# Optimization experiments

Measured on AMD Instinct MI355X. Metric: run time of the kernel, lower is better.

## Reference

```python
import jax, jax.numpy as jnp
import numpy as np
from jax import lax

B, T, I = 8192, 784, 1
H, C = 30, 10


def setup_inputs() -> dict:
    key = jax.random.key(0)
    ks = jax.random.split(key, 6)
    inputs = jax.random.normal(ks[0], (B, T, I), dtype=jnp.float32)
    # RNN cell params (expRNN-style modReLU cell): input kernel (no bias),
    # recurrent kernel (no bias), modReLU bias.
    W_ih = jax.random.normal(ks[1], (H, I), dtype=jnp.float32) / np.sqrt(I)
    W_hh = jax.random.normal(ks[2], (H, H), dtype=jnp.float32) / np.sqrt(H)
    b_mod = jax.random.normal(ks[3], (H,), dtype=jnp.float32) * 0.01
    # Final classifier Linear(hidden_size, num_classes)
    W_lin = jax.random.normal(ks[4], (C, H), dtype=jnp.float32) / np.sqrt(H)
    b_lin = jax.random.normal(ks[5], (C,), dtype=jnp.float32) * 0.01
    return {"inputs": inputs, "W_ih": W_ih, "W_hh": W_hh, "b_mod": b_mod,
            "W_lin": W_lin, "b_lin": b_lin}


def _modrelu(z, b):
    # modReLU: sign(z) * relu(|z| + b)
    return jnp.sign(z) * jax.nn.relu(jnp.abs(z) + b)


def reference(inputs, W_ih, W_hh, b_mod, W_lin, b_lin):
    # inputs: [B, T, 1]; recurrence over T with hidden state [B, H]
    xs = jnp.swapaxes(inputs, 0, 1)  # [T, B, I]

    def step(h, x_t):
        z = x_t @ W_ih.T + h @ W_hh.T  # [B, H]
        h_new = _modrelu(z, b_mod)
        return h_new, None

    h0 = jnp.zeros((inputs.shape[0], W_hh.shape[0]), dtype=inputs.dtype)
    h_final, _ = lax.scan(step, h0, xs)
    return h_final @ W_lin.T + b_lin  # [B, C] logits
```

## Files before the change

### kernel.cpp

```cpp
#include <hip/hip_runtime.h>


#define T_STEPS 784
#define NBATCH  8192
#define NH      30
#define NC      10
#define BPW     16
#define XPAD    788

typedef short bf16x8 __attribute__((ext_vector_type(8)));
typedef float f32x4  __attribute__((ext_vector_type(4)));
typedef unsigned int u32x4 __attribute__((ext_vector_type(4)));

#define MFMA(acc, a, b) \
    acc = __builtin_amdgcn_mfma_f32_16x16x32_bf16(a, b, acc, 0, 0, 0)

__device__ __forceinline__ float truncbf(float x) {
    return __int_as_float(__float_as_int(x) & 0xFFFF0000);
}
__device__ __forceinline__ unsigned pk2(float lo, float hi) {
    return __builtin_amdgcn_perm(__float_as_uint(hi), __float_as_uint(lo),
                                 0x07060302u);
}
__device__ __forceinline__ bf16x8 pk8(float a0, float a1, float a2, float a3,
                                      float a4, float a5, float a6, float a7) {
    u32x4 u = { pk2(a0, a1), pk2(a2, a3), pk2(a4, a5), pk2(a6, a7) };
    return __builtin_bit_cast(bf16x8, u);
}
__device__ __forceinline__ float modrelu(float z, float b) {
    return copysignf(fmaxf(fabsf(z) + b, 0.0f), z);
}

__global__ __launch_bounds__(64, 1)
void rnn_modrelu_mfma2(const float* __restrict__ inp,
                       const float* __restrict__ W_ih,
                       const float* __restrict__ W_hh,
                       const float* __restrict__ b_mod,
                       const float* __restrict__ W_lin,
                       const float* __restrict__ b_lin,
                       float* __restrict__ out)
{
    __shared__ __align__(16) float xl[BPW * XPAD];
    __shared__ float hf[BPW * 32];

    const int l   = threadIdx.x;
    const int blk = blockIdx.x;
    const int m   = l & 15;
    const int q   = l >> 4;

    {
        const float4* src = (const float4*)(inp + (size_t)blk * (BPW * T_STEPS));
        #pragma unroll
        for (int k = 0; k < 49; ++k) {
            int v = l + 64 * k;
            if (v < (BPW * T_STEPS) / 4) {
                int b   = v / 196;
                int rem = v - b * 196;
                *(float4*)(xl + b * XPAD + 4 * rem) = src[v];
            }
        }
    }

    bf16x8 afr[2][3];
    #pragma unroll
    for (int g = 0; g < 2; ++g) {
        const int row = 8 * (m >> 2) + (m & 3) + 4 * g;
        float wv[8], r1v[8], r2v[8];
        #pragma unroll
        for (int j = 0; j < 8; ++j) {
            const int col = q * 8 + j;
            float v = (row < NH && col < NH) ? W_hh[row * NH + col] : 0.0f;
            wv[j]  = v;
            r1v[j] = v - truncbf(v);
            r2v[j] = r1v[j] - truncbf(r1v[j]);
        }
        afr[g][0] = pk8(wv[0],  wv[1],  wv[2],  wv[3],  wv[4],  wv[5],  wv[6],  wv[7]);
        afr[g][1] = pk8(r1v[0], r1v[1], r1v[2], r1v[3], r1v[4], r1v[5], r1v[6], r1v[7]);
        afr[g][2] = pk8(r2v[0], r2v[1], r2v[2], r2v[3], r2v[4], r2v[5], r2v[6], r2v[7]);
    }

    float bm[8], wih[8];
    #pragma unroll
    for (int i = 0; i < 8; ++i) {
        const int row = 8 * q + i;
        bm[i]  = (row < NH) ? b_mod[row] : 0.0f;
        wih[i] = (row < NH) ? W_ih[row]  : 0.0f;
    }

    __syncthreads();

    const float* xb = xl + m * XPAD;
    float xcur = xb[0];
    float xnx  = (T_STEPS > 1) ? xb[1] : xb[0];

    bf16x8 bf1 = {0,0,0,0,0,0,0,0};
    bf16x8 bf2 = {0,0,0,0,0,0,0,0};
    bf16x8 bf3 = {0,0,0,0,0,0,0,0};
    float hv[8];
    #pragma unroll
    for (int i = 0; i < 8; ++i) hv[i] = 0.0f;

    #pragma unroll 1
    for (int t = 0; t < T_STEPS; ++t) {
        int tf = t + 2; if (tf >= T_STEPS) tf = T_STEPS - 1;
        const float xf = xb[tf];

        f32x4 c0, c1;
        #pragma unroll
        for (int i = 0; i < 4; ++i) {
            c0[i] = wih[i]     * xcur;
            c1[i] = wih[4 + i] * xcur;
        }

        MFMA(c0, afr[0][0], bf1);  MFMA(c1, afr[1][0], bf1);
        MFMA(c0, afr[0][1], bf1);  MFMA(c1, afr[1][1], bf1);
        MFMA(c0, afr[0][2], bf1);  MFMA(c1, afr[1][2], bf1);
        MFMA(c0, afr[0][0], bf2);  MFMA(c1, afr[1][0], bf2);
        MFMA(c0, afr[0][1], bf2);  MFMA(c1, afr[1][1], bf2);
        MFMA(c0, afr[0][0], bf3);  MFMA(c1, afr[1][0], bf3);

        #pragma unroll
        for (int i = 0; i < 4; ++i) {
            hv[i]     = modrelu(c0[i], bm[i]);
            hv[4 + i] = modrelu(c1[i], bm[4 + i]);
        }

        float r1[8], r2[8];
        #pragma unroll
        for (int j = 0; j < 8; ++j) {
            r1[j] = hv[j] - truncbf(hv[j]);
            r2[j] = r1[j] - truncbf(r1[j]);
        }
        bf1 = pk8(hv[0], hv[1], hv[2], hv[3], hv[4], hv[5], hv[6], hv[7]);
        bf2 = pk8(r1[0], r1[1], r1[2], r1[3], r1[4], r1[5], r1[6], r1[7]);
        bf3 = pk8(r2[0], r2[1], r2[2], r2[3], r2[4], r2[5], r2[6], r2[7]);

        xcur = xnx;
        xnx  = xf;
    }

    #pragma unroll
    for (int i = 0; i < 8; ++i) {
        const int row = 8 * q + i;
        if (row < NH) hf[m * 32 + row] = hv[i];
    }
    __syncthreads();

    #pragma unroll
    for (int it = 0; it < 3; ++it) {
        const int k = l + 64 * it;
        if (k < BPW * NC) {
            const int b = k / NC;
            const int c = k % NC;
            float acc = b_lin[c];
            #pragma unroll
            for (int i = 0; i < NH; ++i) {
                acc = fmaf(W_lin[c * NH + i], hf[b * 32 + i], acc);
            }
            out[((size_t)blk * BPW + b) * NC + c] = acc;
        }
    }
}

extern "C" void kernel_launch(void* const* d_in, const int* in_sizes, int n_in,
                              void* d_out, int out_size, void* d_ws, size_t ws_size,
                              hipStream_t stream) {
    const float* inp   = (const float*)d_in[0];
    const float* W_ih  = (const float*)d_in[1];
    const float* W_hh  = (const float*)d_in[2];
    const float* b_mod = (const float*)d_in[3];
    const float* W_lin = (const float*)d_in[4];
    const float* b_lin = (const float*)d_in[5];
    float* out = (float*)d_out;

    dim3 grid(NBATCH / BPW);
    dim3 block(64);
    rnn_modrelu_mfma2<<<grid, block, 0, stream>>>(inp, W_ih, W_hh, b_mod,
                                                  W_lin, b_lin, out);
}
```

Measured before the change: 305.0 us.

## Split hidden rows across two waves with LDS exchange of hidden state

```diff
diff --git a/kernel.cpp b/kernel.cpp
--- a/kernel.cpp
+++ b/kernel.cpp
@@ -11,48 +11,52 @@
 typedef short bf16x8 __attribute__((ext_vector_type(8)));
 typedef float f32x4  __attribute__((ext_vector_type(4)));
 typedef unsigned int u32x4 __attribute__((ext_vector_type(4)));
+typedef unsigned int u32x2 __attribute__((ext_vector_type(2)));
 
 #define MFMA(acc, a, b) \
     acc = __builtin_amdgcn_mfma_f32_16x16x32_bf16(a, b, acc, 0, 0, 0)
 
-__device__ __forceinline__ float truncbf(float x) {
+static __device__ __forceinline__ float truncbf(float x) {
     return __int_as_float(__float_as_int(x) & 0xFFFF0000);
 }
-__device__ __forceinline__ unsigned pk2(float lo, float hi) {
+static __device__ __forceinline__ unsigned pk2(float lo, float hi) {
     return __builtin_amdgcn_perm(__float_as_uint(hi), __float_as_uint(lo),
                                  0x07060302u);
 }
-__device__ __forceinline__ bf16x8 pk8(float a0, float a1, float a2, float a3,
-                                      float a4, float a5, float a6, float a7) {
-    u32x4 u = { pk2(a0, a1), pk2(a2, a3), pk2(a4, a5), pk2(a6, a7) };
+static __device__ __forceinline__ bf16x8 pk8(const float* v) {
+    u32x4 u = { pk2(v[0], v[1]), pk2(v[2], v[3]),
+                pk2(v[4], v[5]), pk2(v[6], v[7]) };
     return __builtin_bit_cast(bf16x8, u);
 }
-__device__ __forceinline__ float modrelu(float z, float b) {
+static __device__ __forceinline__ float modrelu(float z, float b) {
     return copysignf(fmaxf(fabsf(z) + b, 0.0f), z);
 }
 
-__global__ __launch_bounds__(64, 1)
-void rnn_modrelu_mfma2(const float* __restrict__ inp,
-                       const float* __restrict__ W_ih,
-                       const float* __restrict__ W_hh,
-                       const float* __restrict__ b_mod,
-                       const float* __restrict__ W_lin,
-                       const float* __restrict__ b_lin,
-                       float* __restrict__ out)
+__global__ __launch_bounds__(128, 1)
+void rnn_rowsplit(const float* __restrict__ inp,
+                  const float* __restrict__ W_ih,
+                  const float* __restrict__ W_hh,
+                  const float* __restrict__ b_mod,
+                  const float* __restrict__ W_lin,
+                  const float* __restrict__ b_lin,
+                  float* __restrict__ out)
 {
     __shared__ __align__(16) float xl[BPW * XPAD];
-    __shared__ float hf[BPW * 32];
+    __shared__ __align__(16) unsigned ex[2][3][4][16][4];
+    __shared__ __align__(16) float hf[BPW * 36];
 
-    const int l   = threadIdx.x;
-    const int blk = blockIdx.x;
+    const int tid = threadIdx.x;
+    const int g   = tid >> 6;
+    const int l   = tid & 63;
     const int m   = l & 15;
     const int q   = l >> 4;
+    const int blk = blockIdx.x;
 
     {
         const float4* src = (const float4*)(inp + (size_t)blk * (BPW * T_STEPS));
         #pragma unroll
-        for (int k = 0; k < 49; ++k) {
-            int v = l + 64 * k;
+        for (int k = 0; k < 25; ++k) {
+            int v = tid + 128 * k;
             if (v < (BPW * T_STEPS) / 4) {
                 int b   = v / 196;
                 int rem = v - b * 196;
@@ -61,9 +65,8 @@
         }
     }
 
-    bf16x8 afr[2][3];
-    #pragma unroll
-    for (int g = 0; g < 2; ++g) {
+    bf16x8 a1, a2, a3;
+    {
         const int row = 8 * (m >> 2) + (m & 3) + 4 * g;
         float wv[8], r1v[8], r2v[8];
         #pragma unroll
@@ -74,15 +77,13 @@
             r1v[j] = v - truncbf(v);
             r2v[j] = r1v[j] - truncbf(r1v[j]);
         }
-        afr[g][0] = pk8(wv[0],  wv[1],  wv[2],  wv[3],  wv[4],  wv[5],  wv[6],  wv[7]);
-        afr[g][1] = pk8(r1v[0], r1v[1], r1v[2], r1v[3], r1v[4], r1v[5], r1v[6], r1v[7]);
-        afr[g][2] = pk8(r2v[0], r2v[1], r2v[2], r2v[3], r2v[4], r2v[5], r2v[6], r2v[7]);
+        a1 = pk8(wv); a2 = pk8(r1v); a3 = pk8(r2v);
     }
 
-    float bm[8], wih[8];
+    float bm[4], wih[4];
     #pragma unroll
-    for (int i = 0; i < 8; ++i) {
-        const int row = 8 * q + i;
+    for (int i = 0; i < 4; ++i) {
+        const int row = 8 * q + 4 * g + i;
         bm[i]  = (row < NH) ? b_mod[row] : 0.0f;
         wih[i] = (row < NH) ? W_ih[row]  : 0.0f;
     }
@@ -91,71 +92,69 @@
 
     const float* xb = xl + m * XPAD;
     float xcur = xb[0];
-    float xnx  = (T_STEPS > 1) ? xb[1] : xb[0];
+    float xnx  = xb[1];
 
-    bf16x8 bf1 = {0,0,0,0,0,0,0,0};
-    bf16x8 bf2 = {0,0,0,0,0,0,0,0};
-    bf16x8 bf3 = {0,0,0,0,0,0,0,0};
-    float hv[8];
-    #pragma unroll
-    for (int i = 0; i < 8; ++i) hv[i] = 0.0f;
+    bf16x8 bf1 = {}, bf2 = {}, bf3 = {};
+    float hv[4] = {0.0f, 0.0f, 0.0f, 0.0f};
 
-    #pragma unroll 1
+    unsigned* const wr0 = &ex[0][0][q][m][2 * g];
+    unsigned* const wr1 = &ex[1][0][q][m][2 * g];
+    const unsigned* const rd0 = &ex[0][0][q][m][0];
+    const unsigned* const rd1 = &ex[1][0][q][m][0];
+
+    #pragma unroll 2
     for (int t = 0; t < T_STEPS; ++t) {
         int tf = t + 2; if (tf >= T_STEPS) tf = T_STEPS - 1;
         const float xf = xb[tf];
 
-        f32x4 c0, c1;
+        f32x4 ca, cb;
+        #pragma unroll
+        for (int i = 0; i < 4; ++i) ca[i] = wih[i] * xcur;
+        cb = (f32x4){0.0f, 0.0f, 0.0f, 0.0f};
+
+        MFMA(ca, a1, bf1);   MFMA(cb, a2, bf1);
+        MFMA(ca, a3, bf1);   MFMA(cb, a1, bf2);
+        MFMA(ca, a2, bf2);   MFMA(cb, a1, bf3);
+
+        #pragma unroll
+        for (int i = 0; i < 4; ++i) hv[i] = modrelu(ca[i] + cb[i], bm[i]);
+
+        float r1[4], r2[4];
         #pragma unroll
         for (int i = 0; i < 4; ++i) {
-            c0[i] = wih[i]     * xcur;
-            c1[i] = wih[4 + i] * xcur;
+            r1[i] = hv[i] - truncbf(hv[i]);
+            r2[i] = r1[i] - truncbf(r1[i]);
         }
 
-        MFMA(c0, afr[0][0], bf1);  MFMA(c1, afr[1][0], bf1);
-        MFMA(c0, afr[0][1], bf1);  MFMA(c1, afr[1][1], bf1);
-        MFMA(c0, afr[0][2], bf1);  MFMA(c1, afr[1][2], bf1);
-        MFMA(c0, afr[0][0], bf2);  MFMA(c1, afr[1][0], bf2);
-        MFMA(c0, afr[0][1], bf2);  MFMA(c1, afr[1][1], bf2);
-        MFMA(c0, afr[0][0], bf3);  MFMA(c1, afr[1][0], bf3);
+        unsigned* w = (t & 1) ? wr1 : wr0;
+        *(u32x2*)(w +   0) = (u32x2){ pk2(hv[0], hv[1]), pk2(hv[2], hv[3]) };
+        *(u32x2*)(w + 256) = (u32x2){ pk2(r1[0], r1[1]), pk2(r1[2], r1[3]) };
+        *(u32x2*)(w + 512) = (u32x2){ pk2(r2[0], r2[1]), pk2(r2[2], r2[3]) };
 
-        #pragma unroll
-        for (int i = 0; i < 4; ++i) {
-            hv[i]     = modrelu(c0[i], bm[i]);
-            hv[4 + i] = modrelu(c1[i], bm[4 + i]);
-        }
+        __syncthreads();
 
-        float r1[8], r2[8];
-        #pragma unroll
-        for (int j = 0; j < 8; ++j) {
-            r1[j] = hv[j] - truncbf(hv[j]);
-            r2[j] = r1[j] - truncbf(r1[j]);
-        }
-        bf1 = pk8(hv[0], hv[1], hv[2], hv[3], hv[4], hv[5], hv[6], hv[7]);
-        bf2 = pk8(r1[0], r1[1], r1[2], r1[3], r1[4], r1[5], r1[6], r1[7]);
-        bf3 = pk8(r2[0], r2[1], r2[2], r2[3], r2[4], r2[5], r2[6], r2[7]);
+        const unsigned* r = (t & 1) ? rd1 : rd0;
+        bf1 = __builtin_bit_cast(bf16x8, *(const u32x4*)(r + 0));
+        bf2 = __builtin_bit_cast(bf16x8, *(const u32x4*)(r + 256));
+        bf3 = __builtin_bit_cast(bf16x8, *(const u32x4*)(r + 512));
 
-        xcur = xnx;
-        xnx  = xf;
+        xcur = xnx; xnx = xf;
     }
 
-    #pragma unroll
-    for (int i = 0; i < 8; ++i) {
-        const int row = 8 * q + i;
-        if (row < NH) hf[m * 32 + row] = hv[i];
-    }
+    *(float4*)(hf + m * 36 + 8 * q + 4 * g) =
+        make_float4(hv[0], hv[1], hv[2], hv[3]);
     __syncthreads();
 
     #pragma unroll
-    for (int it = 0; it < 3; ++it) {
-        const int k = l + 64 * it;
+    for (int it = 0; it < 2; ++it) {
+        const int k = tid + 128 * it;
         if (k < BPW * NC) {
             const int b = k / NC;
             const int c = k % NC;
             float acc = b_lin[c];
             #pragma unroll
             for (int i = 0; i < NH; ++i) {
-                acc = fmaf(W_lin[c * NH + i], hf[b * 32 + i], acc);
+                acc = fmaf(W_lin[c * NH + i], hf[b * 36 + i], acc);
             }
             out[((size_t)blk * BPW + b) * NC + c] = acc;
         }
@@ -174,7 +173,7 @@
     float* out = (float*)d_out;
 
     dim3 grid(NBATCH / BPW);
-    dim3 block(64);
-    rnn_modrelu_mfma2<<<grid, block, 0, stream>>>(inp, W_ih, W_hh, b_mod,
-                                                  W_lin, b_lin, out);
+    dim3 block(128);
+    rnn_rowsplit<<<grid, block, 0, stream>>>(inp, W_ih, W_hh, b_mod,
+                                             W_lin, b_lin, out);
 }
```

New measurement: 266.3 us. 12.7% less time.

## Interleave two batch streams per wave and split MFMA accumulator chains

Applied to the files above, without the earlier changes.

```diff
diff --git a/kernel.cpp b/kernel.cpp
--- a/kernel.cpp
+++ b/kernel.cpp
@@ -5,7 +5,8 @@
 #define NBATCH  8192
 #define NH      30
 #define NC      10
-#define BPW     16
+#define NS      2
+#define BPW     32
 #define XPAD    788
 
 typedef short bf16x8 __attribute__((ext_vector_type(8)));
@@ -15,33 +16,33 @@
 #define MFMA(acc, a, b) \
     acc = __builtin_amdgcn_mfma_f32_16x16x32_bf16(a, b, acc, 0, 0, 0)
 
-__device__ __forceinline__ float truncbf(float x) {
+static __device__ __forceinline__ float truncbf(float x) {
     return __int_as_float(__float_as_int(x) & 0xFFFF0000);
 }
-__device__ __forceinline__ unsigned pk2(float lo, float hi) {
+static __device__ __forceinline__ unsigned pk2(float lo, float hi) {
     return __builtin_amdgcn_perm(__float_as_uint(hi), __float_as_uint(lo),
                                  0x07060302u);
 }
-__device__ __forceinline__ bf16x8 pk8(float a0, float a1, float a2, float a3,
-                                      float a4, float a5, float a6, float a7) {
-    u32x4 u = { pk2(a0, a1), pk2(a2, a3), pk2(a4, a5), pk2(a6, a7) };
+static __device__ __forceinline__ bf16x8 pk8(const float* v) {
+    u32x4 u = { pk2(v[0], v[1]), pk2(v[2], v[3]),
+                pk2(v[4], v[5]), pk2(v[6], v[7]) };
     return __builtin_bit_cast(bf16x8, u);
 }
-__device__ __forceinline__ float modrelu(float z, float b) {
+static __device__ __forceinline__ float modrelu(float z, float b) {
     return copysignf(fmaxf(fabsf(z) + b, 0.0f), z);
 }
 
 __global__ __launch_bounds__(64, 1)
-void rnn_modrelu_mfma2(const float* __restrict__ inp,
-                       const float* __restrict__ W_ih,
-                       const float* __restrict__ W_hh,
-                       const float* __restrict__ b_mod,
-                       const float* __restrict__ W_lin,
-                       const float* __restrict__ b_lin,
-                       float* __restrict__ out)
+void rnn_2stream(const float* __restrict__ inp,
+                 const float* __restrict__ W_ih,
+                 const float* __restrict__ W_hh,
+                 const float* __restrict__ b_mod,
+                 const float* __restrict__ W_lin,
+                 const float* __restrict__ b_lin,
+                 float* __restrict__ out)
 {
     __shared__ __align__(16) float xl[BPW * XPAD];
-    __shared__ float hf[BPW * 32];
+    __shared__ __align__(16) float hf[BPW * 36];
 
     const int l   = threadIdx.x;
     const int blk = blockIdx.x;
@@ -51,13 +52,11 @@
     {
         const float4* src = (const float4*)(inp + (size_t)blk * (BPW * T_STEPS));
         #pragma unroll
-        for (int k = 0; k < 49; ++k) {
+        for (int k = 0; k < 98; ++k) {
             int v = l + 64 * k;
-            if (v < (BPW * T_STEPS) / 4) {
-                int b   = v / 196;
-                int rem = v - b * 196;
-                *(float4*)(xl + b * XPAD + 4 * rem) = src[v];
-            }
+            int b   = v / 196;
+            int rem = v - b * 196;
+            *(float4*)(xl + b * XPAD + 4 * rem) = src[v];
         }
     }
 
@@ -74,9 +73,9 @@
             r1v[j] = v - truncbf(v);
             r2v[j] = r1v[j] - truncbf(r1v[j]);
         }
-        afr[g][0] = pk8(wv[0],  wv[1],  wv[2],  wv[3],  wv[4],  wv[5],  wv[6],  wv[7]);
-        afr[g][1] = pk8(r1v[0], r1v[1], r1v[2], r1v[3], r1v[4], r1v[5], r1v[6], r1v[7]);
-        afr[g][2] = pk8(r2v[0], r2v[1], r2v[2], r2v[3], r2v[4], r2v[5], r2v[6], r2v[7]);
+        afr[g][0] = pk8(wv);
+        afr[g][1] = pk8(r1v);
+        afr[g][2] = pk8(r2v);
     }
 
     float bm[8], wih[8];
@@ -89,76 +88,96 @@
 
     __syncthreads();
 
-    const float* xb = xl + m * XPAD;
-    float xcur = xb[0];
-    float xnx  = (T_STEPS > 1) ? xb[1] : xb[0];
-
-    bf16x8 bf1 = {0,0,0,0,0,0,0,0};
-    bf16x8 bf2 = {0,0,0,0,0,0,0,0};
-    bf16x8 bf3 = {0,0,0,0,0,0,0,0};
-    float hv[8];
+    const float* xb[NS];
+    float xcur[NS], xnx[NS];
+    bf16x8 bf1[NS], bf2[NS], bf3[NS];
+    float hv[NS][8];
     #pragma unroll
-    for (int i = 0; i < 8; ++i) hv[i] = 0.0f;
+    for (int s = 0; s < NS; ++s) {
+        xb[s]   = xl + (16 * s + m) * XPAD;
+        xcur[s] = xb[s][0];
+        xnx[s]  = xb[s][1];
+        bf1[s] = (bf16x8){};
+        bf2[s] = (bf16x8){};
+        bf3[s] = (bf16x8){};
+        #pragma unroll
+        for (int i = 0; i < 8; ++i) hv[s][i] = 0.0f;
+    }
 
     #pragma unroll 1
     for (int t = 0; t < T_STEPS; ++t) {
         int tf = t + 2; if (tf >= T_STEPS) tf = T_STEPS - 1;
-        const float xf = xb[tf];
+        float xf[NS];
+        f32x4 c0a[NS], c0b[NS], c1a[NS], c1b[NS];
 
-        f32x4 c0, c1;
         #pragma unroll
-        for (int i = 0; i < 4; ++i) {
-            c0[i] = wih[i]     * xcur;
-            c1[i] = wih[4 + i] * xcur;
+        for (int s = 0; s < NS; ++s) {
+            xf[s] = xb[s][tf];
+            #pragma unroll
+            for (int i = 0; i < 4; ++i) {
+                c0a[s][i] = wih[i]     * xcur[s];
+                c1a[s][i] = wih[4 + i] * xcur[s];
+            }
+            c0b[s] = (f32x4){0.f, 0.f, 0.f, 0.f};
+            c1b[s] = (f32x4){0.f, 0.f, 0.f, 0.f};
+
+            MFMA(c0a[s], afr[0][0], bf1[s]);
+            MFMA(c1a[s], afr[1][0], bf1[s]);
+            MFMA(c0b[s], afr[0][1], bf1[s]);
+            MFMA(c1b[s], afr[1][1], bf1[s]);
+            MFMA(c0a[s], afr[0][0], bf2[s]);
+            MFMA(c1a[s], afr[1][0], bf2[s]);
+            MFMA(c0b[s], afr[0][1], bf2[s]);
+            MFMA(c1b[s], afr[1][1], bf2[s]);
+            MFMA(c0a[s], afr[0][0], bf3[s]);
+            MFMA(c1a[s], afr[1][0], bf3[s]);
+            MFMA(c0b[s], afr[0][2], bf1[s]);
+            MFMA(c1b[s], afr[1][2], bf1[s]);
         }
 
-        MFMA(c0, afr[0][0], bf1);  MFMA(c1, afr[1][0], bf1);
-        MFMA(c0, afr[0][1], bf1);  MFMA(c1, afr[1][1], bf1);
-        MFMA(c0, afr[0][2], bf1);  MFMA(c1, afr[1][2], bf1);
-        MFMA(c0, afr[0][0], bf2);  MFMA(c1, afr[1][0], bf2);
-        MFMA(c0, afr[0][1], bf2);  MFMA(c1, afr[1][1], bf2);
-        MFMA(c0, afr[0][0], bf3);  MFMA(c1, afr[1][0], bf3);
-
         #pragma unroll
-        for (int i = 0; i < 4; ++i) {
-            hv[i]     = modrelu(c0[i], bm[i]);
-            hv[4 + i] = modrelu(c1[i], bm[4 + i]);
+        for (int s = 0; s < NS; ++s) {
+            #pragma unroll
+            for (int i = 0; i < 4; ++i) {
+                const float z0 = c0a[s][i] + c0b[s][i];
+                const float z1 = c1a[s][i] + c1b[s][i];
+                hv[s][i]     = modrelu(z0, bm[i]);
+                hv[s][4 + i] = modrelu(z1, bm[4 + i]);
+            }
+            float r1[8], r2[8];
+            #pragma unroll
+            for (int j = 0; j < 8; ++j) {
+                r1[j] = hv[s][j] - truncbf(hv[s][j]);
+                r2[j] = r1[j] - truncbf(r1[j]);
+            }
+            bf1[s] = pk8(hv[s]);
+            bf2[s] = pk8(r1);
+            bf3[s] = pk8(r2);
+            xcur[s] = xnx[s];
+            xnx[s]  = xf[s];
         }
-
-        float r1[8], r2[8];
-        #pragma unroll
-        for (int j = 0; j < 8; ++j) {
-            r1[j] = hv[j] - truncbf(hv[j]);
-            r2[j] = r1[j] - truncbf(r1[j]);
-        }
-        bf1 = pk8(hv[0], hv[1], hv[2], hv[3], hv[4], hv[5], hv[6], hv[7]);
-        bf2 = pk8(r1[0], r1[1], r1[2], r1[3], r1[4], r1[5], r1[6], r1[7]);
-        bf3 = pk8(r2[0], r2[1], r2[2], r2[3], r2[4], r2[5], r2[6], r2[7]);
-
-        xcur = xnx;
-        xnx  = xf;
     }
 
     #pragma unroll
-    for (int i = 0; i < 8; ++i) {
-        const int row = 8 * q + i;
-        if (row < NH) hf[m * 32 + row] = hv[i];
+    for (int s = 0; s < NS; ++s) {
+        *(float4*)(hf + (16 * s + m) * 36 + 8 * q) =
+            make_float4(hv[s][0], hv[s][1], hv[s][2], hv[s][3]);
+        *(float4*)(hf + (16 * s + m) * 36 + 8 * q + 4) =
+            make_float4(hv[s][4], hv[s][5], hv[s][6], hv[s][7]);
     }
     __syncthreads();
 
     #pragma unroll
-    for (int it = 0; it < 3; ++it) {
+    for (int it = 0; it < 5; ++it) {
         const int k = l + 64 * it;
-        if (k < BPW * NC) {
-            const int b = k / NC;
-            const int c = k % NC;
-            float acc = b_lin[c];
-            #pragma unroll
-            for (int i = 0; i < NH; ++i) {
-                acc = fmaf(W_lin[c * NH + i], hf[b * 32 + i], acc);
-            }
-            out[((size_t)blk * BPW + b) * NC + c] = acc;
+        const int b = k / NC;
+        const int c = k % NC;
+        float acc = b_lin[c];
+        #pragma unroll
+        for (int i = 0; i < NH; ++i) {
+            acc = fmaf(W_lin[c * NH + i], hf[b * 36 + i], acc);
         }
+        out[((size_t)blk * BPW + b) * NC + c] = acc;
     }
 }
 
@@ -175,6 +194,6 @@
 
     dim3 grid(NBATCH / BPW);
     dim3 block(64);
-    rnn_modrelu_mfma2<<<grid, block, 0, stream>>>(inp, W_ih, W_hh, b_mod,
-                                                  W_lin, b_lin, out);
+    rnn_2stream<<<grid, block, 0, stream>>>(inp, W_ih, W_hh, b_mod,
+                                            W_lin, b_lin, out);
 }
```

New measurement: 505.5 us. +65.8%, slower.
